# Kernel tuning notes

Measured on AMD Instinct MI355X. Metric: run time of the kernel, lower is better.

## Reference

```python
import jax, jax.numpy as jnp
import numpy as np

N = 262144  # points per batch (~4096 rays x 64 samples)
FDIM = 64   # plane feature dim
S = 512     # base plane resolution


def setup_inputs() -> dict:
    key = jax.random.key(0)
    ks = jax.random.split(key, 10)
    x = jax.random.uniform(ks[0], (N, 3), dtype=jnp.float32, minval=-1.0, maxval=1.0)
    rays_o = jnp.array([[0.0, 0.0, 1.5]], dtype=jnp.float32)  # ray origin; distances straddle 1.5/2.0
    scale = jnp.ones((3,), dtype=jnp.float32)
    plane = lambda k, s: jax.random.normal(k, (FDIM, s, s), dtype=jnp.float32)
    return {
        'x': x, 'rays_o': rays_o, 'scale': scale,
        'xy_plane': plane(ks[1], S), 'yz_plane': plane(ks[2], S), 'xz_plane': plane(ks[3], S),
        'xy_plane1': plane(ks[4], S // 2), 'yz_plane1': plane(ks[5], S // 2), 'xz_plane1': plane(ks[6], S // 2),
        'xy_plane2': plane(ks[7], S // 4), 'yz_plane2': plane(ks[8], S // 4), 'xz_plane2': plane(ks[9], S // 4),
    }


def bilinear_sample(plane, coords):
    """F.grid_sample(mode='bilinear', align_corners=True, padding_mode='zeros').
    plane: [C, H, W]; coords: [N, 2] with (x, y) in [-1, 1] (x indexes W).
    Returns [N, C]."""
    C, H, W = plane.shape
    fx = (coords[:, 0] + 1.0) * 0.5 * (W - 1)
    fy = (coords[:, 1] + 1.0) * 0.5 * (H - 1)
    x0 = jnp.floor(fx)
    y0 = jnp.floor(fy)
    wx = fx - x0
    wy = fy - y0
    x0i = x0.astype(jnp.int32)
    y0i = y0.astype(jnp.int32)

    def gather(xi, yi):
        valid = (xi >= 0) & (xi < W) & (yi >= 0) & (yi < H)
        xc = jnp.clip(xi, 0, W - 1)
        yc = jnp.clip(yi, 0, H - 1)
        v = plane[:, yc, xc]  # [C, N]
        return jnp.where(valid[None, :], v, 0.0)

    v00 = gather(x0i, y0i)
    v01 = gather(x0i + 1, y0i)
    v10 = gather(x0i, y0i + 1)
    v11 = gather(x0i + 1, y0i + 1)
    out = (v00 * (1 - wx) * (1 - wy) + v01 * wx * (1 - wy)
           + v10 * (1 - wx) * wy + v11 * wx * wy)  # [C, N]
    return out.T


def forward(x, rays_o, scale, xy0, yz0, xz0, xy1, yz1, xz1, xy2, yz2, xz2):
    xs = x * scale[None, :]
    xy_c = xs[:, :2]                                   # (x, y)
    xz_c = jnp.stack([xs[:, 0], xs[:, 2]], axis=-1)    # (x, z)
    yz_c = xs[:, 1:]                                   # (y, z)

    # laplace breakpoints: first index with distance > 1.5 / > 2.0 from rays_o[0]
    d = jnp.linalg.norm(rays_o[0][None, :] - xs, axis=-1)
    c1 = d > 1.5
    c2 = d > 2.0
    break1 = jnp.where(c1.any(), jnp.argmax(c1), 0)
    break2 = jnp.where(c2.any(), jnp.argmax(c2), 0)
    idx = jnp.arange(x.shape[0])
    # level 0: [0, break1), level 1: [break1, break2), level 2: [break2, N)
    level = jnp.where(idx < break1, 0, jnp.where(idx < break2, 1, 2))[:, None]

    def tri(p0, p1, p2, c):
        s0 = bilinear_sample(p0, c)
        s1 = bilinear_sample(p1, c)
        s2 = bilinear_sample(p2, c)
        # laplace: level1 = fine + half, level2 = fine + half + quarter
        return jnp.where(level == 0, s0, jnp.where(level == 1, s0 + s1, s0 + s1 + s2))

    return (tri(xy0, xy1, xy2, xy_c)
            + tri(xz0, xz1, xz2, xz_c)
            + tri(yz0, yz1, yz2, yz_c))


def reference(x, rays_o, scale, xy_plane, yz_plane, xz_plane, xy_plane1, yz_plane1, xz_plane1, xy_plane2, yz_plane2, xz_plane2):
    return forward(x, rays_o, scale, xy_plane, yz_plane, xz_plane,
                   xy_plane1, yz_plane1, xz_plane1,
                   xy_plane2, yz_plane2, xz_plane2)
```

## Files before the change

kernel.cpp:

```cpp
#include <hip/hip_runtime.h>
#include <hip/hip_fp16.h>

#define NPTS 262144
#define FDIM 64
#define NCELL 32768

typedef float vfloat4 __attribute__((ext_vector_type(4)));

__global__ __launch_bounds__(256) void break_kernel(const float* __restrict__ x,
                                                    const float* __restrict__ rays_o,
                                                    const float* __restrict__ scale,
                                                    unsigned* __restrict__ breaks) {
  const unsigned t = blockIdx.x * 256u + threadIdx.x;
  const float r0 = rays_o[0], r1 = rays_o[1], r2 = rays_o[2];
  const float s0 = scale[0], s1 = scale[1], s2 = scale[2];
  unsigned b1 = 0xFFFFFFFFu, b2 = 0xFFFFFFFFu;
  for (unsigned p = t; p < NPTS; p += 65536u) {
    const float dx = r0 - x[p * 3 + 0] * s0;
    const float dy = r1 - x[p * 3 + 1] * s1;
    const float dz = r2 - x[p * 3 + 2] * s2;
    const float d = sqrtf(__fadd_rn(__fadd_rn(__fmul_rn(dx, dx), __fmul_rn(dy, dy)),
                                    __fmul_rn(dz, dz)));
    if (d > 1.5f) b1 = min(b1, p);
    if (d > 2.0f) b2 = min(b2, p);
  }
  __shared__ unsigned sb1[256];
  __shared__ unsigned sb2[256];
  sb1[threadIdx.x] = b1;
  sb2[threadIdx.x] = b2;
  __syncthreads();
  for (int s = 128; s > 0; s >>= 1) {
    if ((int)threadIdx.x < s) {
      sb1[threadIdx.x] = min(sb1[threadIdx.x], sb1[threadIdx.x + s]);
      sb2[threadIdx.x] = min(sb2[threadIdx.x], sb2[threadIdx.x + s]);
    }
    __syncthreads();
  }
  if (threadIdx.x == 0) {
    atomicMin(&breaks[0], sb1[0]);
    atomicMin(&breaks[1], sb2[0]);
  }
}

__device__ __forceinline__ unsigned part5(unsigned v) {
  v &= 31u;
  v = (v | (v << 8)) & 0x100Fu;
  v = (v | (v << 4)) & 0x10C3u;
  v = (v | (v << 2)) & 0x1249u;
  return v;
}

__device__ __forceinline__ unsigned cell_key(float x0, float x1, float x2) {
  const int cx = min(max((int)((x0 + 1.0f) * 16.0f), 0), 31);
  const int cy = min(max((int)((x1 + 1.0f) * 16.0f), 0), 31);
  const int cz = min(max((int)((x2 + 1.0f) * 16.0f), 0), 31);
  return part5((unsigned)cx) | (part5((unsigned)cy) << 1) | (part5((unsigned)cz) << 2);
}

__global__ __launch_bounds__(256) void hist_kernel(const float* __restrict__ x,
                                                   const float* __restrict__ scale,
                                                   unsigned* __restrict__ hist) {
  const unsigned t = blockIdx.x * 256u + threadIdx.x;
  const float s0 = scale[0], s1 = scale[1], s2 = scale[2];
  const unsigned key = cell_key(x[t * 3 + 0] * s0, x[t * 3 + 1] * s1, x[t * 3 + 2] * s2);
  atomicAdd(&hist[key], 1u);
}

__global__ __launch_bounds__(256) void scan_kernel(unsigned* __restrict__ hist) {
  const int tid = threadIdx.x;
  unsigned s = 0;
  for (int i = 0; i < 128; ++i) s += hist[tid * 128 + i];
  __shared__ unsigned ls[256];
  ls[tid] = s;
  __syncthreads();
  for (int d = 1; d < 256; d <<= 1) {
    const unsigned add = (tid >= d) ? ls[tid - d] : 0u;
    __syncthreads();
    ls[tid] += add;
    __syncthreads();
  }
  unsigned run = ls[tid] - s;
  for (int i = 0; i < 128; ++i) {
    const unsigned h = hist[tid * 128 + i];
    hist[tid * 128 + i] = run;
    run += h;
  }
}

__global__ __launch_bounds__(256) void scatter_kernel(const float* __restrict__ x,
                                                      const float* __restrict__ scale,
                                                      unsigned* __restrict__ offs,
                                                      unsigned* __restrict__ order) {
  const unsigned t = blockIdx.x * 256u + threadIdx.x;
  const float s0 = scale[0], s1 = scale[1], s2 = scale[2];
  const unsigned key = cell_key(x[t * 3 + 0] * s0, x[t * 3 + 1] * s1, x[t * 3 + 2] * s2);
  const unsigned pos = atomicAdd(&offs[key], 1u);
  order[pos] = t;
}

struct TransposeArgs {
  const float* src[9];
  __half* dst[9];
  int tile_hi[9];
  int SS[9];
};

__global__ __launch_bounds__(256) void transpose_all(TransposeArgs a) {
  __shared__ __half lds[64 * 66];
  const int tile = blockIdx.x;
  int pi = 0;
#pragma unroll
  for (int i = 0; i < 9; ++i) {
    if (tile >= a.tile_hi[i]) pi = i + 1;
  }
  const int lo = (pi == 0) ? 0 : a.tile_hi[pi - 1];
  const float* __restrict__ src = a.src[pi];
  __half* __restrict__ dst = a.dst[pi];
  const size_t SS = (size_t)a.SS[pi];
  const size_t p0 = (size_t)(tile - lo) * 64;

  const int t = threadIdx.x;
  const int px4 = t & 15;
  const int cg = t >> 4;
#pragma unroll
  for (int it = 0; it < 4; ++it) {
    const int c = it * 16 + cg;
    const float4 v = *(const float4*)(src + (size_t)c * SS + p0 + (size_t)px4 * 4);
    lds[(px4 * 4 + 0) * 66 + c] = __float2half(v.x);
    lds[(px4 * 4 + 1) * 66 + c] = __float2half(v.y);
    lds[(px4 * 4 + 2) * 66 + c] = __float2half(v.z);
    lds[(px4 * 4 + 3) * 66 + c] = __float2half(v.w);
  }
  __syncthreads();
  const int c8 = t & 7;
  const int pxo = t >> 3;
#pragma unroll
  for (int it = 0; it < 2; ++it) {
    const int px = it * 32 + pxo;
    const unsigned* w = (const unsigned*)(lds + px * 66 + c8 * 8);
    uint4 v;
    v.x = w[0]; v.y = w[1]; v.z = w[2]; v.w = w[3];
    *(uint4*)(dst + (p0 + (size_t)px) * FDIM + c8 * 8) = v;
  }
}

union H8 { uint4 u; __half h[8]; };

__device__ __forceinline__ void bilinear_weights(int W, float cx, float cy,
                                                 float& w00, float& w01, float& w10, float& w11,
                                                 int& xc0, int& xc1, int& yc0, int& yc1) {
  const float Wm1 = (float)(W - 1);
  const float fx = (cx + 1.0f) * 0.5f * Wm1;
  const float fy = (cy + 1.0f) * 0.5f * Wm1;
  const float x0f = floorf(fx), y0f = floorf(fy);
  const float wx = fx - x0f, wy = fy - y0f;
  const int ix = (int)x0f, iy = (int)y0f;
  const int ix1 = ix + 1, iy1 = iy + 1;
  const bool vx0 = (ix >= 0) && (ix < W);
  const bool vx1 = (ix1 >= 0) && (ix1 < W);
  const bool vy0 = (iy >= 0) && (iy < W);
  const bool vy1 = (iy1 >= 0) && (iy1 < W);
  xc0 = min(max(ix, 0), W - 1);
  xc1 = min(max(ix1, 0), W - 1);
  yc0 = min(max(iy, 0), W - 1);
  yc1 = min(max(iy1, 0), W - 1);
  w00 = (1.0f - wx) * (1.0f - wy) * (float)(vx0 && vy0);
  w01 = wx * (1.0f - wy) * (float)(vx1 && vy0);
  w10 = (1.0f - wx) * wy * (float)(vx0 && vy1);
  w11 = wx * wy * (float)(vx1 && vy1);
}

__device__ __forceinline__ void sample8_t(const __half* __restrict__ pl, int W,
                                          float cx, float cy, int j8, float acc[8]) {
  float w00, w01, w10, w11;
  int xc0, xc1, yc0, yc1;
  bilinear_weights(W, cx, cy, w00, w01, w10, w11, xc0, xc1, yc0, yc1);
  const __half* b00 = pl + ((size_t)(yc0 * W + xc0) * FDIM + j8);
  const __half* b01 = pl + ((size_t)(yc0 * W + xc1) * FDIM + j8);
  const __half* b10 = pl + ((size_t)(yc1 * W + xc0) * FDIM + j8);
  const __half* b11 = pl + ((size_t)(yc1 * W + xc1) * FDIM + j8);
  H8 v00, v01, v10, v11;
  v00.u = *(const uint4*)b00;
  v01.u = *(const uint4*)b01;
  v10.u = *(const uint4*)b10;
  v11.u = *(const uint4*)b11;
#pragma unroll
  for (int k = 0; k < 8; ++k) {
    acc[k] += w00 * __half2float(v00.h[k]) + w01 * __half2float(v01.h[k]) +
              w10 * __half2float(v10.h[k]) + w11 * __half2float(v11.h[k]);
  }
}

__device__ __forceinline__ void sample8_d(const float* __restrict__ pl, int W,
                                          float cx, float cy, int j8, float acc[8]) {
  float w00, w01, w10, w11;
  int xc0, xc1, yc0, yc1;
  bilinear_weights(W, cx, cy, w00, w01, w10, w11, xc0, xc1, yc0, yc1);
  const size_t SS = (size_t)W * W;
  const int i00 = yc0 * W + xc0, i01 = yc0 * W + xc1;
  const int i10 = yc1 * W + xc0, i11 = yc1 * W + xc1;
#pragma unroll
  for (int k = 0; k < 8; ++k) {
    const size_t co = (size_t)(j8 + k) * SS;
    acc[k] += w00 * pl[co + i00] + w01 * pl[co + i01] +
              w10 * pl[co + i10] + w11 * pl[co + i11];
  }
}

struct PlanesH { const __half* p[9]; };
struct PlanesF { const float* p[9]; };

__global__ __launch_bounds__(256) void sample_kernel(const float* __restrict__ x,
                                                     const float* __restrict__ scale,
                                                     const unsigned* __restrict__ breaks,
                                                     const unsigned* __restrict__ order,
                                                     PlanesH tp, float* __restrict__ out) {
  const int t = blockIdx.x * 256 + threadIdx.x;
  const int slot = t >> 3;
  const int p = (int)order[slot];
  const int j8 = (t & 7) * 8;
  const float s0 = scale[0], s1 = scale[1], s2 = scale[2];
  const float xs0 = x[p * 3 + 0] * s0;
  const float xs1 = x[p * 3 + 1] * s1;
  const float xs2 = x[p * 3 + 2] * s2;
  unsigned b1 = breaks[0]; if (b1 >= NPTS) b1 = 0;
  unsigned b2 = breaks[1]; if (b2 >= NPTS) b2 = 0;
  const unsigned pu = (unsigned)p;
  const int level = (pu < b1) ? 0 : ((pu < b2) ? 1 : 2);
  float acc[8];
#pragma unroll
  for (int k = 0; k < 8; ++k) acc[k] = 0.0f;
  sample8_t(tp.p[0], 512, xs0, xs1, j8, acc);
  sample8_t(tp.p[1], 512, xs1, xs2, j8, acc);
  sample8_t(tp.p[2], 512, xs0, xs2, j8, acc);
  if (level >= 1) {
    sample8_t(tp.p[3], 256, xs0, xs1, j8, acc);
    sample8_t(tp.p[4], 256, xs1, xs2, j8, acc);
    sample8_t(tp.p[5], 256, xs0, xs2, j8, acc);
  }
  if (level >= 2) {
    sample8_t(tp.p[6], 128, xs0, xs1, j8, acc);
    sample8_t(tp.p[7], 128, xs1, xs2, j8, acc);
    sample8_t(tp.p[8], 128, xs0, xs2, j8, acc);
  }
  float* o = out + (size_t)p * FDIM + j8;
  vfloat4 lo = {acc[0], acc[1], acc[2], acc[3]};
  vfloat4 hi = {acc[4], acc[5], acc[6], acc[7]};
  __builtin_nontemporal_store(lo, (vfloat4*)o);
  __builtin_nontemporal_store(hi, (vfloat4*)(o + 4));
}

__global__ __launch_bounds__(256) void sample_kernel_direct(const float* __restrict__ x,
                                                            const float* __restrict__ scale,
                                                            const unsigned* __restrict__ breaks,
                                                            PlanesF tp, float* __restrict__ out) {
  const int t = blockIdx.x * 256 + threadIdx.x;
  const int p = t >> 3;
  const int j8 = (t & 7) * 8;
  const float s0 = scale[0], s1 = scale[1], s2 = scale[2];
  const float xs0 = x[p * 3 + 0] * s0;
  const float xs1 = x[p * 3 + 1] * s1;
  const float xs2 = x[p * 3 + 2] * s2;
  unsigned b1 = breaks[0]; if (b1 >= NPTS) b1 = 0;
  unsigned b2 = breaks[1]; if (b2 >= NPTS) b2 = 0;
  const unsigned pu = (unsigned)p;
  const int level = (pu < b1) ? 0 : ((pu < b2) ? 1 : 2);
  float acc[8];
#pragma unroll
  for (int k = 0; k < 8; ++k) acc[k] = 0.0f;
  sample8_d(tp.p[0], 512, xs0, xs1, j8, acc);
  sample8_d(tp.p[1], 512, xs1, xs2, j8, acc);
  sample8_d(tp.p[2], 512, xs0, xs2, j8, acc);
  if (level >= 1) {
    sample8_d(tp.p[3], 256, xs0, xs1, j8, acc);
    sample8_d(tp.p[4], 256, xs1, xs2, j8, acc);
    sample8_d(tp.p[5], 256, xs0, xs2, j8, acc);
  }
  if (level >= 2) {
    sample8_d(tp.p[6], 128, xs0, xs1, j8, acc);
    sample8_d(tp.p[7], 128, xs1, xs2, j8, acc);
    sample8_d(tp.p[8], 128, xs0, xs2, j8, acc);
  }
  float4* o4 = (float4*)(out + (size_t)p * FDIM + j8);
  o4[0] = make_float4(acc[0], acc[1], acc[2], acc[3]);
  o4[1] = make_float4(acc[4], acc[5], acc[6], acc[7]);
}

extern "C" void kernel_launch(void* const* d_in, const int* in_sizes, int n_in,
                              void* d_out, int out_size, void* d_ws, size_t ws_size,
                              hipStream_t stream) {
  const float* x = (const float*)d_in[0];
  const float* rays_o = (const float*)d_in[1];
  const float* scale = (const float*)d_in[2];
  const float* pl32[9];
  for (int i = 0; i < 9; ++i) pl32[i] = (const float*)d_in[3 + i];
  float* out = (float*)d_out;

  unsigned char* ws = (unsigned char*)d_ws;
  unsigned* breaks = (unsigned*)ws;
  unsigned* hist = (unsigned*)(ws + 256);
  unsigned* order = (unsigned*)(ws + 256 + NCELL * 4);
  const size_t planes_off = 256 + (size_t)NCELL * 4 + (size_t)NPTS * 4;

  (void)hipMemsetAsync(d_ws, 0xFF, 8, stream);
  break_kernel<<<256, 256, 0, stream>>>(x, rays_o, scale, breaks);

  const int Ss[3] = {512, 256, 128};
  size_t need = planes_off;
  for (int l = 0; l < 3; ++l) need += 3 * (size_t)Ss[l] * Ss[l] * FDIM * sizeof(__half);

  if (ws_size >= need) {
    (void)hipMemsetAsync(hist, 0, NCELL * 4, stream);
    hist_kernel<<<NPTS / 256, 256, 0, stream>>>(x, scale, hist);
    scan_kernel<<<1, 256, 0, stream>>>(hist);
    scatter_kernel<<<NPTS / 256, 256, 0, stream>>>(x, scale, hist, order);

    PlanesH tp;
    TransposeArgs ta;
    size_t off = planes_off;
    int tiles_acc = 0;
    for (int l = 0; l < 3; ++l) {
      const int S = Ss[l];
      const int SS = S * S;
      for (int o = 0; o < 3; ++o) {
        const int i = l * 3 + o;
        __half* dst = (__half*)(ws + off);
        tp.p[i] = dst;
        ta.src[i] = pl32[i];
        ta.dst[i] = dst;
        ta.SS[i] = SS;
        tiles_acc += SS / 64;
        ta.tile_hi[i] = tiles_acc;
        off += (size_t)SS * FDIM * sizeof(__half);
      }
    }
    transpose_all<<<tiles_acc, 256, 0, stream>>>(ta);
    sample_kernel<<<(NPTS * 8) / 256, 256, 0, stream>>>(x, scale, breaks, order, tp, out);
  } else {
    PlanesF tf;
    for (int i = 0; i < 9; ++i) tf.p[i] = pl32[i];
    sample_kernel_direct<<<(NPTS * 8) / 256, 256, 0, stream>>>(x, scale, breaks, tf, out);
  }
}
```

Before: 437.8 us.

## Parallelize histogram scan across blocks and enlarge transpose tiles

```diff
diff --git a/kernel.cpp b/kernel.cpp
--- a/kernel.cpp
+++ b/kernel.cpp
@@ -66,12 +66,13 @@
   atomicAdd(&hist[key], 1u);
 }
 
-__global__ __launch_bounds__(256) void scan_kernel(unsigned* __restrict__ hist) {
+__global__ __launch_bounds__(256) void scan1_kernel(unsigned* __restrict__ hist,
+                                                    unsigned* __restrict__ partials) {
+  const int cell = blockIdx.x * 256 + threadIdx.x;
   const int tid = threadIdx.x;
-  unsigned s = 0;
-  for (int i = 0; i < 128; ++i) s += hist[tid * 128 + i];
+  const unsigned h = hist[cell];
   __shared__ unsigned ls[256];
-  ls[tid] = s;
+  ls[tid] = h;
   __syncthreads();
   for (int d = 1; d < 256; d <<= 1) {
     const unsigned add = (tid >= d) ? ls[tid - d] : 0u;
@@ -79,12 +80,29 @@
     ls[tid] += add;
     __syncthreads();
   }
-  unsigned run = ls[tid] - s;
-  for (int i = 0; i < 128; ++i) {
-    const unsigned h = hist[tid * 128 + i];
-    hist[tid * 128 + i] = run;
-    run += h;
-  }
+  hist[cell] = ls[tid] - h;
+  if (tid == 255) partials[blockIdx.x] = ls[255];
+}
+
+__global__ __launch_bounds__(128) void scan2_kernel(unsigned* __restrict__ partials) {
+  const int tid = threadIdx.x;
+  const unsigned h = partials[tid];
+  __shared__ unsigned ls[128];
+  ls[tid] = h;
+  __syncthreads();
+  for (int d = 1; d < 128; d <<= 1) {
+    const unsigned add = (tid >= d) ? ls[tid - d] : 0u;
+    __syncthreads();
+    ls[tid] += add;
+    __syncthreads();
+  }
+  partials[tid] = ls[tid] - h;
+}
+
+__global__ __launch_bounds__(256) void scan3_kernel(unsigned* __restrict__ hist,
+                                                    const unsigned* __restrict__ partials) {
+  const int cell = blockIdx.x * 256 + threadIdx.x;
+  hist[cell] += partials[blockIdx.x];
 }
 
 __global__ __launch_bounds__(256) void scatter_kernel(const float* __restrict__ x,
@@ -106,7 +124,7 @@
 };
 
 __global__ __launch_bounds__(256) void transpose_all(TransposeArgs a) {
-  __shared__ __half lds[64 * 66];
+  __shared__ __half lds[256 * 66];
   const int tile = blockIdx.x;
   int pi = 0;
 #pragma unroll
@@ -117,14 +135,14 @@
   const float* __restrict__ src = a.src[pi];
   __half* __restrict__ dst = a.dst[pi];
   const size_t SS = (size_t)a.SS[pi];
-  const size_t p0 = (size_t)(tile - lo) * 64;
+  const size_t p0 = (size_t)(tile - lo) * 256;
 
   const int t = threadIdx.x;
-  const int px4 = t & 15;
-  const int cg = t >> 4;
-#pragma unroll
-  for (int it = 0; it < 4; ++it) {
-    const int c = it * 16 + cg;
+  const int px4 = t & 63;
+  const int cg = t >> 6;
+#pragma unroll
+  for (int it = 0; it < 16; ++it) {
+    const int c = it * 4 + cg;
     const float4 v = *(const float4*)(src + (size_t)c * SS + p0 + (size_t)px4 * 4);
     lds[(px4 * 4 + 0) * 66 + c] = __float2half(v.x);
     lds[(px4 * 4 + 1) * 66 + c] = __float2half(v.y);
@@ -135,7 +153,7 @@
   const int c8 = t & 7;
   const int pxo = t >> 3;
 #pragma unroll
-  for (int it = 0; it < 2; ++it) {
+  for (int it = 0; it < 8; ++it) {
     const int px = it * 32 + pxo;
     const unsigned* w = (const unsigned*)(lds + px * 66 + c8 * 8);
     uint4 v;
@@ -298,9 +316,10 @@
 
   unsigned char* ws = (unsigned char*)d_ws;
   unsigned* breaks = (unsigned*)ws;
-  unsigned* hist = (unsigned*)(ws + 256);
-  unsigned* order = (unsigned*)(ws + 256 + NCELL * 4);
-  const size_t planes_off = 256 + (size_t)NCELL * 4 + (size_t)NPTS * 4;
+  unsigned* partials = (unsigned*)(ws + 128);
+  unsigned* hist = (unsigned*)(ws + 1024);
+  unsigned* order = (unsigned*)(ws + 1024 + NCELL * 4);
+  const size_t planes_off = 1024 + (size_t)NCELL * 4 + (size_t)NPTS * 4;
 
   (void)hipMemsetAsync(d_ws, 0xFF, 8, stream);
   break_kernel<<<256, 256, 0, stream>>>(x, rays_o, scale, breaks);
@@ -312,7 +331,9 @@
   if (ws_size >= need) {
     (void)hipMemsetAsync(hist, 0, NCELL * 4, stream);
     hist_kernel<<<NPTS / 256, 256, 0, stream>>>(x, scale, hist);
-    scan_kernel<<<1, 256, 0, stream>>>(hist);
+    scan1_kernel<<<NCELL / 256, 256, 0, stream>>>(hist, partials);
+    scan2_kernel<<<1, 128, 0, stream>>>(partials);
+    scan3_kernel<<<NCELL / 256, 256, 0, stream>>>(hist, partials);
     scatter_kernel<<<NPTS / 256, 256, 0, stream>>>(x, scale, hist, order);
 
     PlanesH tp;
@@ -329,7 +350,7 @@
         ta.src[i] = pl32[i];
         ta.dst[i] = dst;
         ta.SS[i] = SS;
-        tiles_acc += SS / 64;
+        tiles_acc += SS / 256;
         ta.tile_hi[i] = tiles_acc;
         off += (size_t)SS * FDIM * sizeof(__half);
       }
```

New measurement: 429.0 us. -2.0%, faster.
